# Optimization experiments

Hardware: AMD Instinct MI355X
Metric: run time of the kernel (lower is better)

Reference implementation:

```python
import jax, jax.numpy as jnp
import numpy as np

TRIANGLE_TABLE = jnp.array([
    [-1,-1,-1,-1,-1,-1],[1,0,2,-1,-1,-1],[4,0,3,-1,-1,-1],[1,4,2,1,3,4],
    [3,1,5,-1,-1,-1],[2,3,0,2,5,3],[1,4,0,1,5,4],[4,2,5,-1,-1,-1],
    [4,5,2,-1,-1,-1],[4,1,0,4,5,1],[3,2,0,3,5,2],[1,3,5,-1,-1,-1],
    [4,1,2,4,3,1],[3,0,4,-1,-1,-1],[2,0,1,-1,-1,-1],[-1,-1,-1,-1,-1,-1]], dtype=jnp.int32)
NUM_TRI_TABLE = jnp.array([0,1,1,2,1,2,2,1,1,2,2,1,2,1,1,0], dtype=jnp.int32)
BASE_TET_EDGES = jnp.array([0,1,0,2,0,3,1,2,1,3,2,3], dtype=jnp.int32)
N_VERTS, N_TETS = 200_000, 1_000_000


def setup_inputs() -> dict:
    key = jax.random.key(0)
    k1, k2, k3 = jax.random.split(key, 3)
    pos_nx3 = jax.random.normal(k1, (N_VERTS, 3), jnp.float32)
    sdf_n = jax.random.normal(k2, (N_VERTS,), jnp.float32)
    tet_fx4 = jax.random.randint(k3, (N_TETS, 4), 0, N_VERTS, dtype=jnp.int32)
    return {"pos_nx3": pos_nx3, "sdf_n": sdf_n, "tet_fx4": tet_fx4}


def _mt_indices(sdf_n, tet_fx4):
    # Index-only part (torch.no_grad in the original). Dynamic shapes -> eager jax.
    occ_n = sdf_n > 0                              # [N]
    occ_fx4 = occ_n[tet_fx4]                       # [T,4]
    occ_sum = occ_fx4.sum(-1)
    valid = (occ_sum > 0) & (occ_sum < 4)          # surface-crossing tets
    tets_v = tet_fx4[valid]                        # [Tv,4]
    occ_v = occ_fx4[valid]
    # 6 edges per tet, sorted so (min,max) -> dedup identical to torch sort_edges+unique
    all_edges = jnp.sort(tets_v[:, BASE_TET_EDGES].reshape(-1, 2), axis=1)  # [Tv*6,2]
    unique_edges, idx_map = jnp.unique(all_edges, axis=0, return_inverse=True)
    idx_map = idx_map.reshape(-1)
    mask_edges = occ_n[unique_edges].sum(-1) == 1  # exactly one endpoint inside
    # compacting map: -1 for non-crossing edges, running index for crossing ones
    mapping = jnp.where(mask_edges, jnp.cumsum(mask_edges.astype(jnp.int32)) - 1, -1)
    idx_map = mapping[idx_map].reshape(-1, 6)      # [Tv,6] per-tet edge->vertex ids
    interp_v = unique_edges[mask_edges]            # [Ne,2] endpoint indices
    return valid, occ_v, idx_map, interp_v


def _interp_verts(pos, sdf, interp_v):
    e_pos = pos[interp_v]                                   # [Ne,2,3]
    e_sdf = sdf[interp_v] * jnp.array([1.0, -1.0], sdf.dtype)  # [s0,-s1]
    denom = e_sdf.sum(1, keepdims=True)                     # s0 - s1
    w = e_sdf[:, ::-1] / denom                              # [-s1, s0] / (s0-s1)
    return (e_pos * w[..., None]).sum(1)                    # [Ne,3]


def _map_uv(face_gidx, max_idx):
    Ngrid = int(np.ceil(np.sqrt((max_idx + 1) // 2)))
    lin = jnp.linspace(0.0, 1.0 - 1.0 / Ngrid, Ngrid, dtype=jnp.float32)
    tex_y, tex_x = jnp.meshgrid(lin, lin, indexing='ij')
    pad = 0.9 / Ngrid
    uvs = jnp.stack([tex_x, tex_y, tex_x + pad, tex_y,
                     tex_x + pad, tex_y + pad, tex_x, tex_y + pad], axis=-1).reshape(-1, 2)
    tet_raw = face_gidx // 2
    tet_idx = (tet_raw // Ngrid) * Ngrid + tet_raw % Ngrid
    tri_idx = face_gidx % 2
    uv_idx = jnp.stack([tet_idx * 4, tet_idx * 4 + tri_idx + 1,
                        tet_idx * 4 + tri_idx + 2], axis=-1).reshape(-1, 3)
    return uvs, uv_idx


def reference(pos_nx3, sdf_n, tet_fx4):
    valid, occ_v, idx_map, interp_v = _mt_indices(sdf_n, tet_fx4)
    verts = _interp_verts(pos_nx3, sdf_n, interp_v)
    # triangle-table lookup
    v_id = jnp.array([1, 2, 4, 8], jnp.int32)
    tetindex = (occ_v.astype(jnp.int32) * v_id).sum(-1)     # [Tv]
    num_tri = NUM_TRI_TABLE[tetindex]
    m1, m2 = num_tri == 1, num_tri == 2
    faces1 = jnp.take_along_axis(idx_map[m1], TRIANGLE_TABLE[tetindex[m1]][:, :3], axis=1).reshape(-1, 3)
    faces2 = jnp.take_along_axis(idx_map[m2], TRIANGLE_TABLE[tetindex[m2]][:, :6], axis=1).reshape(-1, 3)
    faces = jnp.concatenate([faces1, faces2], axis=0)
    tet_gidx = jnp.nonzero(valid)[0].astype(jnp.int32)
    face_gidx = jnp.concatenate([
        tet_gidx[m1] * 2,
        jnp.stack([tet_gidx[m2] * 2, tet_gidx[m2] * 2 + 1], axis=-1).reshape(-1)], axis=0)
    uvs, uv_idx = _map_uv(face_gidx, tet_fx4.shape[0] * 2)
    return verts, faces, uvs, uv_idx
```

## Files before the change

kernel.cpp:

```cpp
#include <hip/hip_runtime.h>
#include <cmath>

typedef unsigned long long u64;
typedef unsigned int u32;
typedef unsigned char u8;

#define SCAN_BLOCK 256
#define SCAN_ELEMS 8
#define SCAN_TILE (SCAN_BLOCK * SCAN_ELEMS)

#define BIN_SHIFT 9
#define BIN_VR 512
#define TETS_PER_BLOCK 2048

__constant__ int d_NUMTRI[16] = {0,1,1,2,1,2,2,1,1,2,2,1,2,1,1,0};
__constant__ int d_TRI[16][6] = {
 {-1,-1,-1,-1,-1,-1},{1,0,2,-1,-1,-1},{4,0,3,-1,-1,-1},{1,4,2,1,3,4},
 {3,1,5,-1,-1,-1},{2,3,0,2,5,3},{1,4,0,1,5,4},{4,2,5,-1,-1,-1},
 {4,5,2,-1,-1,-1},{4,1,0,4,5,1},{3,2,0,3,5,2},{1,3,5,-1,-1,-1},
 {4,1,2,4,3,1},{3,0,4,-1,-1,-1},{2,0,1,-1,-1,-1},{-1,-1,-1,-1,-1,-1}};
__constant__ int d_E0[6] = {0,0,0,1,1,2};
__constant__ int d_E1[6] = {1,2,3,2,3,3};

template <typename T>
__global__ void scanA_t(const T* in, T* out, int n, T* blockSums) {
    __shared__ T tsum[SCAN_BLOCK];
    int tbase = blockIdx.x * SCAN_TILE + threadIdx.x * SCAN_ELEMS;
    T vals[SCAN_ELEMS];
    T run = 0;
    for (int k = 0; k < SCAN_ELEMS; ++k) {
        int i = tbase + k;
        T v = (i < n) ? in[i] : (T)0;
        vals[k] = run;
        run += v;
    }
    tsum[threadIdx.x] = run;
    __syncthreads();
    for (int off = 1; off < SCAN_BLOCK; off <<= 1) {
        T v = (threadIdx.x >= (unsigned)off) ? tsum[threadIdx.x - off] : (T)0;
        __syncthreads();
        tsum[threadIdx.x] += v;
        __syncthreads();
    }
    T texcl = (threadIdx.x == 0) ? (T)0 : tsum[threadIdx.x - 1];
    for (int k = 0; k < SCAN_ELEMS; ++k) {
        int i = tbase + k;
        if (i < n) out[i] = texcl + vals[k];
    }
    if (threadIdx.x == SCAN_BLOCK - 1) blockSums[blockIdx.x] = tsum[SCAN_BLOCK - 1];
}

template <typename T>
__global__ void scanB_t(T* bs, int nb, T* totalOut) {
    __shared__ T sh[2048];
    for (int i = threadIdx.x; i < 2048; i += 256) sh[i] = (i < nb) ? bs[i] : (T)0;
    __syncthreads();
    for (int off = 1; off < 2048; off <<= 1) {
        T v[8];
        for (int k = 0; k < 8; ++k) {
            int i = threadIdx.x + k * 256;
            v[k] = (i >= off) ? sh[i - off] : (T)0;
        }
        __syncthreads();
        for (int k = 0; k < 8; ++k) sh[threadIdx.x + k * 256] += v[k];
        __syncthreads();
    }
    for (int i = threadIdx.x; i < nb; i += 256) bs[i] = (i == 0) ? (T)0 : sh[i - 1];
    if (threadIdx.x == 0 && totalOut) *totalOut = (nb > 0) ? sh[nb - 1] : (T)0;
}

template <typename T>
__global__ void scanC_t(T* out, int n, const T* bs) {
    int base = blockIdx.x * SCAN_TILE;
    T add = bs[blockIdx.x];
    int end = base + SCAN_TILE; if (end > n) end = n;
    for (int i = base + threadIdx.x; i < end; i += SCAN_BLOCK) out[i] += add;
}

__global__ __launch_bounds__(256) void k_classify_hist(
    const int* tet, const float* sdf, u8* ti8, u64* tetPack,
    u32* blockHist, int T, int NB, int gB) {
    __shared__ u32 hist[BIN_VR];
    for (int i = threadIdx.x; i < NB; i += 256) hist[i] = 0;
    __syncthreads();
    int base = blockIdx.x * TETS_PER_BLOCK;
    for (int it = 0; it < TETS_PER_BLOCK / 256; ++it) {
        int t = base + it * 256 + threadIdx.x;
        if (t < T) {
            int4 q = reinterpret_cast<const int4*>(tet)[t];
            int ti = (sdf[q.x] > 0.0f ? 1 : 0) | (sdf[q.y] > 0.0f ? 2 : 0) |
                     (sdf[q.z] > 0.0f ? 4 : 0) | (sdf[q.w] > 0.0f ? 8 : 0);
            ti8[t] = (u8)ti;
            int nt = d_NUMTRI[ti];
            tetPack[t] = ((u64)(nt == 1 ? 1 : 0) << 21) | (u64)(nt == 2 ? 1 : 0);
            if (nt != 0) {
                int idx[4] = {q.x, q.y, q.z, q.w};
                #pragma unroll
                for (int e = 0; e < 6; ++e) {
                    int e0 = d_E0[e], e1 = d_E1[e];
                    if (((ti >> e0) ^ (ti >> e1)) & 1) {
                        int a = idx[e0], b = idx[e1];
                        int mn = a < b ? a : b;
                        atomicAdd(&hist[mn >> BIN_SHIFT], 1u);
                    }
                }
            }
        }
    }
    __syncthreads();
    for (int i = threadIdx.x; i < NB; i += 256)
        blockHist[(size_t)i * gB + blockIdx.x] = hist[i];
}

__global__ __launch_bounds__(256) void k_binfill(
    const int* tet, const u8* ti8, const u32* blockHistScan,
    u32* binData, int T, int NB, int gB) {
    __shared__ u32 cur[BIN_VR];
    for (int i = threadIdx.x; i < NB; i += 256)
        cur[i] = blockHistScan[(size_t)i * gB + blockIdx.x];
    __syncthreads();
    int base = blockIdx.x * TETS_PER_BLOCK;
    for (int it = 0; it < TETS_PER_BLOCK / 256; ++it) {
        int t = base + it * 256 + threadIdx.x;
        if (t < T) {
            int ti = ti8[t];
            if (d_NUMTRI[ti] != 0) {
                int4 q = reinterpret_cast<const int4*>(tet)[t];
                int idx[4] = {q.x, q.y, q.z, q.w};
                #pragma unroll
                for (int e = 0; e < 6; ++e) {
                    int e0 = d_E0[e], e1 = d_E1[e];
                    if (((ti >> e0) ^ (ti >> e1)) & 1) {
                        int a = idx[e0], b = idx[e1];
                        int mn = a < b ? a : b;
                        int mx = a < b ? b : a;
                        u32 slot = atomicAdd(&cur[mn >> BIN_SHIFT], 1u);
                        binData[slot] = ((u32)(mn & (BIN_VR - 1)) << 18) | (u32)mx;
                    }
                }
            }
        }
    }
}

__global__ __launch_bounds__(256) void k_bincount(
    const u32* blockHistScan, const u32* totalPtr, const u32* binData,
    u32* bucketCnt, u32* padCnt, int V, int NB, int gB) {
    int bin = blockIdx.x;
    __shared__ u32 hist[BIN_VR];
    for (int i = threadIdx.x; i < BIN_VR; i += 256) hist[i] = 0;
    __syncthreads();
    u32 s = blockHistScan[(size_t)bin * gB];
    u32 e = (bin + 1 < NB) ? blockHistScan[(size_t)(bin + 1) * gB] : *totalPtr;
    for (u32 i = s + threadIdx.x; i < e; i += 256)
        atomicAdd(&hist[binData[i] >> 18], 1u);
    __syncthreads();
    int vbase = bin << BIN_SHIFT;
    for (int i = threadIdx.x; i < BIN_VR; i += 256) {
        int v = vbase + i;
        if (v < V) {
            u32 h = hist[i];
            bucketCnt[v] = h;
            padCnt[v] = (h + 15u) & ~15u;
        }
    }
}

__global__ __launch_bounds__(256) void k_binscatter(
    const u32* blockHistScan, const u32* totalPtr, const u32* binData,
    const u32* bucketStart, u32* maxArr, int V, int NB, int gB) {
    int bin = blockIdx.x;
    __shared__ u32 cur[BIN_VR];
    int vbase = bin << BIN_SHIFT;
    for (int i = threadIdx.x; i < BIN_VR; i += 256) {
        int v = vbase + i;
        cur[i] = (v < V) ? bucketStart[v] : 0u;
    }
    __syncthreads();
    u32 s = blockHistScan[(size_t)bin * gB];
    u32 e = (bin + 1 < NB) ? blockHistScan[(size_t)(bin + 1) * gB] : *totalPtr;
    for (u32 i = s + threadIdx.x; i < e; i += 256) {
        u32 rec = binData[i];
        u32 slot = atomicAdd(&cur[rec >> 18], 1u);
        maxArr[slot] = rec & 0x3FFFFu;
    }
}

__global__ __launch_bounds__(64) void k_sortdedup(
    const u32* bucketCnt, const u32* bucketStart, u32* maxArr, u32* crossCnt, int V)
{
    int v = blockIdx.x;
    if (v >= V) return;
    int lane = threadIdx.x;
    int n = (int)bucketCnt[v];
    if (n == 0) { if (lane == 0) crossCnt[v] = 0; return; }
    long long start = (long long)bucketStart[v];

    if (n <= 64) {
        u32 key = (lane < n) ? maxArr[start + lane] : 0xFFFFFFFFu;
        int rank = 0;
        for (int j = 0; j < n; ++j) {
            u32 kj = (u32)__shfl((int)key, j);
            rank += (kj < key || (kj == key && j < lane)) ? 1 : 0;
        }
        u32 sorted = (u32)__builtin_amdgcn_ds_permute(rank << 2, (int)key);
        u32 prev = (u32)__shfl((int)sorted, lane - 1);
        bool nf = (lane < n) && (lane == 0 || prev != sorted);
        u64 m = __ballot(nf);
        int idx = __popcll(m & ((1ull << lane) - 1ull));
        if (nf) maxArr[start + idx] = sorted;
        if (lane == 0) crossCnt[v] = (u32)__popcll(m);
    } else if (n <= 256) {
        __shared__ u32 sk[256];
        __shared__ u32 ss[256];
        int chunks = (n + 63) >> 6;
        u32 key[4];
        #pragma unroll
        for (int c = 0; c < 4; ++c) {
            if (c < chunks) {
                int i = (c << 6) + lane;
                key[c] = (i < n) ? maxArr[start + i] : 0xFFFFFFFFu;
                sk[(c << 6) + lane] = key[c];
            }
        }
        __syncthreads();
        int rank[4] = {0, 0, 0, 0};
        for (int j = 0; j < n; ++j) {
            u32 kj = sk[j];
            #pragma unroll
            for (int c = 0; c < 4; ++c) {
                if (c < chunks) {
                    int i = (c << 6) + lane;
                    rank[c] += (kj < key[c] || (kj == key[c] && j < i)) ? 1 : 0;
                }
            }
        }
        #pragma unroll
        for (int c = 0; c < 4; ++c) {
            if (c < chunks) { int i = (c << 6) + lane; if (i < n) ss[rank[c]] = key[c]; }
        }
        __syncthreads();
        int carryU = 0;
        for (int c = 0; c < chunks; ++c) {
            int i = (c << 6) + lane;
            bool valid = i < n;
            u32 k = ss[i < 256 ? i : 255];
            bool nf = valid && (i == 0 || ss[i - 1] != k);
            u64 mnf = __ballot(nf);
            u64 incl = (2ull << lane) - 1ull;
            int uIncl = carryU + __popcll(mnf & incl);
            if (nf) maxArr[start + uIncl - 1] = k;
            carryU += __popcll(mnf);
        }
        if (lane == 0) crossCnt[v] = (u32)carryU;
    } else if (lane == 0) {
        for (int i = 1; i < n; ++i) {
            u32 kk = maxArr[start + i];
            int j = i - 1;
            while (j >= 0 && maxArr[start + j] > kk) {
                maxArr[start + j + 1] = maxArr[start + j]; --j;
            }
            maxArr[start + j + 1] = kk;
        }
        int uc = 0; u32 prev = 0xFFFFFFFFu;
        for (int i = 0; i < n; ++i) {
            u32 k = maxArr[start + i];
            if (k != prev) { maxArr[start + uc] = k; ++uc; prev = k; }
        }
        crossCnt[v] = (u32)uc;
    }
}

__global__ void k_metapack(const u32* bucketStart, const u32* crossCnt,
                           const u32* crossScan, uint2* meta2, int V) {
    int v = blockIdx.x * 256 + threadIdx.x;
    if (v < V) meta2[v] = make_uint2(bucketStart[v], (crossCnt[v] << 22) | crossScan[v]);
}

__global__ __launch_bounds__(64) void k_verts(
    const u32* crossCnt, const u32* bucketStart, const u32* maxArr, const u32* crossScan,
    const float* pos, const float* sdf, float* out, int V)
{
    int v = blockIdx.x;
    if (v >= V) return;
    int lane = threadIdx.x;
    int u = (int)crossCnt[v];
    if (u == 0) return;
    long long start = (long long)bucketStart[v];
    int cBase = (int)crossScan[v];
    float s0 = sdf[v];
    float p0x = pos[3 * v], p0y = pos[3 * v + 1], p0z = pos[3 * v + 2];
    for (int i = lane; i < u; i += 64) {
        int b = (int)maxArr[start + i];
        long long k = cBase + i;
        float s1 = sdf[b];
        float d = s0 - s1;
        float w0 = -s1 / d, w1 = s0 / d;
        out[3 * k + 0] = p0x * w0 + pos[3 * b + 0] * w1;
        out[3 * k + 1] = p0y * w0 + pos[3 * b + 1] * w1;
        out[3 * k + 2] = p0z * w0 + pos[3 * b + 2] * w1;
    }
}

__global__ void k_faces(const int* tet, const u8* ti8, const u64* tetScan,
                        const uint2* meta2, const u32* maxArr,
                        const u64* meta0, const u32* NePtr,
                        float* out, int T, int Ngrid, long long uvFloats)
{
    int t = blockIdx.x * 256 + threadIdx.x;
    if (t >= T) return;
    int ti = ti8[t];
    int nt = d_NUMTRI[ti];
    if (nt == 0) return;

    u64 tot = *meta0;
    int C1 = (int)((tot >> 21) & 0x1fffffull);
    int C2 = (int)(tot & 0x1fffffull);
    int Ne = (int)*NePtr;
    long long facesBase = 3LL * Ne;
    long long F = (long long)C1 + 2LL * C2;
    long long uvIdxBase = facesBase + 3LL * F + uvFloats;

    int4 q = reinterpret_cast<const int4*>(tet)[t];
    int idx[4] = {q.x, q.y, q.z, q.w};
    const int* row = d_TRI[ti];

    int emap[6];
    unsigned done = 0;
    float fv[6];
    #pragma unroll
    for (int j = 0; j < 6; ++j) {
        if (j >= 3 * nt) break;
        int e = row[j];
        if (!((done >> e) & 1)) {
            done |= 1u << e;
            int a = idx[d_E0[e]], b = idx[d_E1[e]];
            if (a > b) { int tmp = a; a = b; b = tmp; }
            uint2 m = meta2[a];
            int u = (int)(m.y >> 22);
            int base = (int)(m.y & 0x3FFFFFu);
            const uint4* bp = (const uint4*)(maxArr + m.x);
            int cnt = 0;
            int nv = (u + 3) >> 2;
            for (int k4 = 0; k4 < nv; ++k4) {
                uint4 w = bp[k4];
                int b4 = k4 << 2;
                cnt += (b4 + 0 < u && (int)w.x < b) ? 1 : 0;
                cnt += (b4 + 1 < u && (int)w.y < b) ? 1 : 0;
                cnt += (b4 + 2 < u && (int)w.z < b) ? 1 : 0;
                cnt += (b4 + 3 < u && (int)w.w < b) ? 1 : 0;
            }
            emap[e] = base + cnt;
        }
        fv[j] = (float)emap[e];
    }

    u64 sc = tetScan[t];
    int r1 = (int)((sc >> 21) & 0x1fffffull);
    int r2 = (int)(sc & 0x1fffffull);
    int tet_idx = (t / Ngrid) * Ngrid + (t % Ngrid);

    if (nt == 1) {
        long long f = r1;
        out[facesBase + 3 * f + 0] = fv[0];
        out[facesBase + 3 * f + 1] = fv[1];
        out[facesBase + 3 * f + 2] = fv[2];
        out[uvIdxBase + 3 * f + 0] = (float)(4 * tet_idx);
        out[uvIdxBase + 3 * f + 1] = (float)(4 * tet_idx + 1);
        out[uvIdxBase + 3 * f + 2] = (float)(4 * tet_idx + 2);
    } else {
        long long f0 = (long long)C1 + 2LL * r2;
        out[facesBase + 3 * f0 + 0] = fv[0];
        out[facesBase + 3 * f0 + 1] = fv[1];
        out[facesBase + 3 * f0 + 2] = fv[2];
        out[facesBase + 3 * (f0 + 1) + 0] = fv[3];
        out[facesBase + 3 * (f0 + 1) + 1] = fv[4];
        out[facesBase + 3 * (f0 + 1) + 2] = fv[5];
        out[uvIdxBase + 3 * f0 + 0] = (float)(4 * tet_idx);
        out[uvIdxBase + 3 * f0 + 1] = (float)(4 * tet_idx + 1);
        out[uvIdxBase + 3 * f0 + 2] = (float)(4 * tet_idx + 2);
        out[uvIdxBase + 3 * (f0 + 1) + 0] = (float)(4 * tet_idx);
        out[uvIdxBase + 3 * (f0 + 1) + 1] = (float)(4 * tet_idx + 2);
        out[uvIdxBase + 3 * (f0 + 1) + 2] = (float)(4 * tet_idx + 3);
    }
}

__global__ void k_uvs(float* out, const u64* meta0, const u32* NePtr, int Ngrid) {
    int c = blockIdx.x * 256 + threadIdx.x;
    int total = Ngrid * Ngrid;
    if (c >= total) return;
    u64 tot = *meta0;
    int C1 = (int)((tot >> 21) & 0x1fffffull);
    int C2 = (int)(tot & 0x1fffffull);
    int Ne = (int)*NePtr;
    long long uvBase = 3LL * Ne + 3LL * ((long long)C1 + 2LL * C2);
    int i = c / Ngrid, j = c % Ngrid;
    double step = (Ngrid > 1) ? (1.0 - 1.0 / (double)Ngrid) / (double)(Ngrid - 1) : 0.0;
    float x = (float)((double)j * step);
    float y = (float)((double)i * step);
    float pad = (float)(0.9 / (double)Ngrid);
    long long o = uvBase + 8LL * c;
    out[o + 0] = x;       out[o + 1] = y;
    out[o + 2] = x + pad; out[o + 3] = y;
    out[o + 4] = x + pad; out[o + 5] = y + pad;
    out[o + 6] = x;       out[o + 7] = y + pad;
}

template <typename T>
static void run_scan_t(const T* in, T* out, int n, T* blockSums, T* totalOut,
                       hipStream_t stream) {
    int nb = (n + SCAN_TILE - 1) / SCAN_TILE;
    scanA_t<T><<<nb, SCAN_BLOCK, 0, stream>>>(in, out, n, blockSums);
    scanB_t<T><<<1, 256, 0, stream>>>(blockSums, nb, totalOut);
    scanC_t<T><<<nb, SCAN_BLOCK, 0, stream>>>(out, n, blockSums);
}

extern "C" void kernel_launch(void* const* d_in, const int* in_sizes, int n_in,
                              void* d_out, int out_size, void* d_ws, size_t ws_size,
                              hipStream_t stream) {
    const float* pos = (const float*)d_in[0];
    const float* sdf = (const float*)d_in[1];
    const int* tet = (const int*)d_in[2];
    int V = in_sizes[1];
    int T = in_sizes[2] / 4;
    float* out = (float*)d_out;

    int NB = (V + BIN_VR - 1) / BIN_VR;
    int gB = (T + TETS_PER_BLOCK - 1) / TETS_PER_BLOCK;
    int nHist = NB * gB;

    char* p = (char*)d_ws;
    auto alloc = [&](size_t bytes) -> void* {
        void* r = (void*)p;
        p += (bytes + 255) & ~(size_t)255;
        return r;
    };
    u8*  ti8           = (u8*) alloc((size_t)T);
    u64* tetPack       = (u64*)alloc((size_t)T * 8);
    u64* tetScan       = (u64*)alloc((size_t)T * 8);
    u32* blockHist     = (u32*)alloc((size_t)nHist * 4);
    u32* blockHistScan = (u32*)alloc((size_t)nHist * 4);
    u32* binData       = (u32*)alloc((size_t)6 * T * 4);
    u32* bucketCnt     = (u32*)alloc((size_t)V * 4);
    u32* padCnt        = (u32*)alloc((size_t)V * 4);
    u32* bucketStart   = (u32*)alloc((size_t)V * 4);
    u32* crossCnt      = (u32*)alloc((size_t)V * 4);
    u32* crossScan     = (u32*)alloc((size_t)V * 4);
    uint2* meta2       = (uint2*)alloc((size_t)V * 8);
    u32* maxArr        = (u32*)alloc(((size_t)6 * T + 16 * (size_t)V) * 4);
    u64* blockSums64   = (u64*)alloc(2048 * 8);
    u32* blockSums32   = (u32*)alloc(2048 * 4);
    u64* meta64        = (u64*)alloc(8 * 8);
    u32* NePtr         = (u32*)(meta64 + 4);
    u32* NeInstPtr     = (u32*)(meta64 + 5);

    long long M = (2LL * T + 1) / 2;
    int Ngrid = (int)std::sqrt((double)M);
    while ((long long)Ngrid * Ngrid < M) ++Ngrid;
    if (Ngrid < 1) Ngrid = 1;
    long long uvFloats = 8LL * Ngrid * Ngrid;

    int gV = (V + 255) / 256;
    int gT = (T + 255) / 256;

    k_classify_hist<<<gB, 256, 0, stream>>>(tet, sdf, ti8, tetPack, blockHist,
                                            T, NB, gB);
    run_scan_t<u64>(tetPack, tetScan, T, blockSums64, meta64, stream);
    run_scan_t<u32>(blockHist, blockHistScan, nHist, blockSums32, NeInstPtr, stream);
    k_binfill<<<gB, 256, 0, stream>>>(tet, ti8, blockHistScan, binData, T, NB, gB);
    k_bincount<<<NB, 256, 0, stream>>>(blockHistScan, NeInstPtr, binData,
                                       bucketCnt, padCnt, V, NB, gB);
    run_scan_t<u32>(padCnt, bucketStart, V, blockSums32, nullptr, stream);
    k_binscatter<<<NB, 256, 0, stream>>>(blockHistScan, NeInstPtr, binData,
                                         bucketStart, maxArr, V, NB, gB);
    k_sortdedup<<<V, 64, 0, stream>>>(bucketCnt, bucketStart, maxArr, crossCnt, V);
    run_scan_t<u32>(crossCnt, crossScan, V, blockSums32, NePtr, stream);
    k_metapack<<<gV, 256, 0, stream>>>(bucketStart, crossCnt, crossScan, meta2, V);
    k_verts<<<V, 64, 0, stream>>>(crossCnt, bucketStart, maxArr, crossScan,
                                  pos, sdf, out, V);
    k_faces<<<gT, 256, 0, stream>>>(tet, ti8, tetScan, meta2, maxArr,
                                    meta64, NePtr, out, T, Ngrid, uvFloats);
    int gUV = (Ngrid * Ngrid + 255) / 256;
    k_uvs<<<gUV, 256, 0, stream>>>(out, meta64, NePtr, Ngrid);
}
```

Baseline: 500.5 us.

## Track edge provenance through binning to build direct per-tet edge index map

Each crossing edge record now carries a provenance id (tet*6+edge) through binfill and binscatter. The sort/dedup kernel uses it to write each edge's local unique index into an idxmap laid over the binData buffer. k_faces then reads the six entries per tet directly instead of linearly scanning each vertex's sorted bucket, and the metapack kernel is removed. In exchange it adds extra global writes and reads for provenance, scattered nontemporal stores, and raises the shared-sort path limit to 1024 elements with larger register arrays.

```diff
diff --git a/kernel.cpp b/kernel.cpp
--- a/kernel.cpp
+++ b/kernel.cpp
@@ -114,7 +114,7 @@
 
 __global__ __launch_bounds__(256) void k_binfill(
     const int* tet, const u8* ti8, const u32* blockHistScan,
-    u32* binData, int T, int NB, int gB) {
+    u32* binData, u32* binProv, int T, int NB, int gB) {
     __shared__ u32 cur[BIN_VR];
     for (int i = threadIdx.x; i < NB; i += 256)
         cur[i] = blockHistScan[(size_t)i * gB + blockIdx.x];
@@ -136,6 +136,7 @@
                         int mx = a < b ? b : a;
                         u32 slot = atomicAdd(&cur[mn >> BIN_SHIFT], 1u);
                         binData[slot] = ((u32)(mn & (BIN_VR - 1)) << 18) | (u32)mx;
+                        binProv[slot] = 6u * (u32)t + (u32)e;
                     }
                 }
             }
@@ -168,7 +169,8 @@
 
 __global__ __launch_bounds__(256) void k_binscatter(
     const u32* blockHistScan, const u32* totalPtr, const u32* binData,
-    const u32* bucketStart, u32* maxArr, int V, int NB, int gB) {
+    const u32* binProv, const u32* bucketStart, u32* maxArr, u32* provArr,
+    int V, int NB, int gB) {
     int bin = blockIdx.x;
     __shared__ u32 cur[BIN_VR];
     int vbase = bin << BIN_SHIFT;
@@ -181,13 +183,16 @@
     u32 e = (bin + 1 < NB) ? blockHistScan[(size_t)(bin + 1) * gB] : *totalPtr;
     for (u32 i = s + threadIdx.x; i < e; i += 256) {
         u32 rec = binData[i];
+        u32 pv = binProv[i];
         u32 slot = atomicAdd(&cur[rec >> 18], 1u);
         maxArr[slot] = rec & 0x3FFFFu;
+        provArr[slot] = pv;
     }
 }
 
 __global__ __launch_bounds__(64) void k_sortdedup(
-    const u32* bucketCnt, const u32* bucketStart, u32* maxArr, u32* crossCnt, int V)
+    const u32* bucketCnt, const u32* bucketStart, u32* maxArr,
+    u32* provArr, u32* idxmap, u32* crossCnt, int V)
 {
     int v = blockIdx.x;
     if (v >= V) return;
@@ -198,6 +203,7 @@
 
     if (n <= 64) {
         u32 key = (lane < n) ? maxArr[start + lane] : 0xFFFFFFFFu;
+        u32 prov = (lane < n) ? provArr[start + lane] : 0u;
         int rank = 0;
         for (int j = 0; j < n; ++j) {
             u32 kj = (u32)__shfl((int)key, j);
@@ -209,26 +215,32 @@
         u64 m = __ballot(nf);
         int idx = __popcll(m & ((1ull << lane) - 1ull));
         if (nf) maxArr[start + idx] = sorted;
+        int ldSorted = nf ? idx : idx - 1;
+        int ldOrig = __shfl(ldSorted, rank);
+        if (lane < n)
+            __builtin_nontemporal_store((u32)ldOrig, &idxmap[prov]);
         if (lane == 0) crossCnt[v] = (u32)__popcll(m);
-    } else if (n <= 256) {
-        __shared__ u32 sk[256];
-        __shared__ u32 ss[256];
+    } else if (n <= 1024) {
+        __shared__ u32 sk[1024];
+        __shared__ u32 ss[1024];
+        __shared__ u32 sdd[1024];
         int chunks = (n + 63) >> 6;
-        u32 key[4];
+        u32 key[16];
+        int rank[16];
         #pragma unroll
-        for (int c = 0; c < 4; ++c) {
+        for (int c = 0; c < 16; ++c) {
             if (c < chunks) {
                 int i = (c << 6) + lane;
                 key[c] = (i < n) ? maxArr[start + i] : 0xFFFFFFFFu;
                 sk[(c << 6) + lane] = key[c];
+                rank[c] = 0;
             }
         }
         __syncthreads();
-        int rank[4] = {0, 0, 0, 0};
         for (int j = 0; j < n; ++j) {
             u32 kj = sk[j];
             #pragma unroll
-            for (int c = 0; c < 4; ++c) {
+            for (int c = 0; c < 16; ++c) {
                 if (c < chunks) {
                     int i = (c << 6) + lane;
                     rank[c] += (kj < key[c] || (kj == key[c] && j < i)) ? 1 : 0;
@@ -236,7 +248,7 @@
             }
         }
         #pragma unroll
-        for (int c = 0; c < 4; ++c) {
+        for (int c = 0; c < 16; ++c) {
             if (c < chunks) { int i = (c << 6) + lane; if (i < n) ss[rank[c]] = key[c]; }
         }
         __syncthreads();
@@ -244,37 +256,48 @@
         for (int c = 0; c < chunks; ++c) {
             int i = (c << 6) + lane;
             bool valid = i < n;
-            u32 k = ss[i < 256 ? i : 255];
+            u32 k = ss[valid ? i : n - 1];
             bool nf = valid && (i == 0 || ss[i - 1] != k);
             u64 mnf = __ballot(nf);
             u64 incl = (2ull << lane) - 1ull;
             int uIncl = carryU + __popcll(mnf & incl);
             if (nf) maxArr[start + uIncl - 1] = k;
+            if (valid) sdd[i] = (u32)(uIncl - 1);
             carryU += __popcll(mnf);
+        }
+        __syncthreads();
+        #pragma unroll
+        for (int c = 0; c < 16; ++c) {
+            if (c < chunks) {
+                int i = (c << 6) + lane;
+                if (i < n)
+                    __builtin_nontemporal_store(sdd[rank[c]],
+                                                &idxmap[provArr[start + i]]);
+            }
         }
         if (lane == 0) crossCnt[v] = (u32)carryU;
     } else if (lane == 0) {
         for (int i = 1; i < n; ++i) {
             u32 kk = maxArr[start + i];
+            u32 pp = provArr[start + i];
             int j = i - 1;
             while (j >= 0 && maxArr[start + j] > kk) {
-                maxArr[start + j + 1] = maxArr[start + j]; --j;
+                maxArr[start + j + 1] = maxArr[start + j];
+                provArr[start + j + 1] = provArr[start + j];
+                --j;
             }
             maxArr[start + j + 1] = kk;
+            provArr[start + j + 1] = pp;
         }
         int uc = 0; u32 prev = 0xFFFFFFFFu;
         for (int i = 0; i < n; ++i) {
             u32 k = maxArr[start + i];
             if (k != prev) { maxArr[start + uc] = k; ++uc; prev = k; }
+            __builtin_nontemporal_store((u32)(uc - 1),
+                                        &idxmap[provArr[start + i]]);
         }
         crossCnt[v] = (u32)uc;
     }
-}
-
-__global__ void k_metapack(const u32* bucketStart, const u32* crossCnt,
-                           const u32* crossScan, uint2* meta2, int V) {
-    int v = blockIdx.x * 256 + threadIdx.x;
-    if (v < V) meta2[v] = make_uint2(bucketStart[v], (crossCnt[v] << 22) | crossScan[v]);
 }
 
 __global__ __launch_bounds__(64) void k_verts(
@@ -303,7 +326,7 @@
 }
 
 __global__ void k_faces(const int* tet, const u8* ti8, const u64* tetScan,
-                        const uint2* meta2, const u32* maxArr,
+                        const u32* idxmap, const u32* crossScan,
                         const u64* meta0, const u32* NePtr,
                         float* out, int T, int Ngrid, long long uvFloats)
 {
@@ -323,6 +346,9 @@
 
     int4 q = reinterpret_cast<const int4*>(tet)[t];
     int idx[4] = {q.x, q.y, q.z, q.w};
+    const uint2* imp = reinterpret_cast<const uint2*>(idxmap + 6ll * t);
+    uint2 r0 = imp[0], r1 = imp[1], r2 = imp[2];
+    u32 im[6] = {r0.x, r0.y, r1.x, r1.y, r2.x, r2.y};
     const int* row = d_TRI[ti];
 
     int emap[6];
@@ -335,33 +361,19 @@
         if (!((done >> e) & 1)) {
             done |= 1u << e;
             int a = idx[d_E0[e]], b = idx[d_E1[e]];
-            if (a > b) { int tmp = a; a = b; b = tmp; }
-            uint2 m = meta2[a];
-            int u = (int)(m.y >> 22);
-            int base = (int)(m.y & 0x3FFFFFu);
-            const uint4* bp = (const uint4*)(maxArr + m.x);
-            int cnt = 0;
-            int nv = (u + 3) >> 2;
-            for (int k4 = 0; k4 < nv; ++k4) {
-                uint4 w = bp[k4];
-                int b4 = k4 << 2;
-                cnt += (b4 + 0 < u && (int)w.x < b) ? 1 : 0;
-                cnt += (b4 + 1 < u && (int)w.y < b) ? 1 : 0;
-                cnt += (b4 + 2 < u && (int)w.z < b) ? 1 : 0;
-                cnt += (b4 + 3 < u && (int)w.w < b) ? 1 : 0;
-            }
-            emap[e] = base + cnt;
+            if (b < a) a = b;
+            emap[e] = (int)crossScan[a] + (int)im[e];
         }
         fv[j] = (float)emap[e];
     }
 
     u64 sc = tetScan[t];
-    int r1 = (int)((sc >> 21) & 0x1fffffull);
-    int r2 = (int)(sc & 0x1fffffull);
+    int r1s = (int)((sc >> 21) & 0x1fffffull);
+    int r2s = (int)(sc & 0x1fffffull);
     int tet_idx = (t / Ngrid) * Ngrid + (t % Ngrid);
 
     if (nt == 1) {
-        long long f = r1;
+        long long f = r1s;
         out[facesBase + 3 * f + 0] = fv[0];
         out[facesBase + 3 * f + 1] = fv[1];
         out[facesBase + 3 * f + 2] = fv[2];
@@ -369,7 +381,7 @@
         out[uvIdxBase + 3 * f + 1] = (float)(4 * tet_idx + 1);
         out[uvIdxBase + 3 * f + 2] = (float)(4 * tet_idx + 2);
     } else {
-        long long f0 = (long long)C1 + 2LL * r2;
+        long long f0 = (long long)C1 + 2LL * r2s;
         out[facesBase + 3 * f0 + 0] = fv[0];
         out[facesBase + 3 * f0 + 1] = fv[1];
         out[facesBase + 3 * f0 + 2] = fv[2];
@@ -441,44 +453,48 @@
     u32* blockHist     = (u32*)alloc((size_t)nHist * 4);
     u32* blockHistScan = (u32*)alloc((size_t)nHist * 4);
     u32* binData       = (u32*)alloc((size_t)6 * T * 4);
+    u32* binProv       = (u32*)alloc((size_t)6 * T * 4);
     u32* bucketCnt     = (u32*)alloc((size_t)V * 4);
     u32* padCnt        = (u32*)alloc((size_t)V * 4);
     u32* bucketStart   = (u32*)alloc((size_t)V * 4);
     u32* crossCnt      = (u32*)alloc((size_t)V * 4);
     u32* crossScan     = (u32*)alloc((size_t)V * 4);
-    uint2* meta2       = (uint2*)alloc((size_t)V * 8);
     u32* maxArr        = (u32*)alloc(((size_t)6 * T + 16 * (size_t)V) * 4);
+    u32* provArr       = (u32*)alloc(((size_t)6 * T + 16 * (size_t)V) * 4);
     u64* blockSums64   = (u64*)alloc(2048 * 8);
     u32* blockSums32   = (u32*)alloc(2048 * 4);
     u64* meta64        = (u64*)alloc(8 * 8);
     u32* NePtr         = (u32*)(meta64 + 4);
     u32* NeInstPtr     = (u32*)(meta64 + 5);
 
+    u32* idxmap = binData;
+
     long long M = (2LL * T + 1) / 2;
     int Ngrid = (int)std::sqrt((double)M);
     while ((long long)Ngrid * Ngrid < M) ++Ngrid;
     if (Ngrid < 1) Ngrid = 1;
     long long uvFloats = 8LL * Ngrid * Ngrid;
 
-    int gV = (V + 255) / 256;
     int gT = (T + 255) / 256;
 
     k_classify_hist<<<gB, 256, 0, stream>>>(tet, sdf, ti8, tetPack, blockHist,
                                             T, NB, gB);
     run_scan_t<u64>(tetPack, tetScan, T, blockSums64, meta64, stream);
     run_scan_t<u32>(blockHist, blockHistScan, nHist, blockSums32, NeInstPtr, stream);
-    k_binfill<<<gB, 256, 0, stream>>>(tet, ti8, blockHistScan, binData, T, NB, gB);
+    k_binfill<<<gB, 256, 0, stream>>>(tet, ti8, blockHistScan, binData, binProv,
+                                      T, NB, gB);
     k_bincount<<<NB, 256, 0, stream>>>(blockHistScan, NeInstPtr, binData,
                                        bucketCnt, padCnt, V, NB, gB);
     run_scan_t<u32>(padCnt, bucketStart, V, blockSums32, nullptr, stream);
     k_binscatter<<<NB, 256, 0, stream>>>(blockHistScan, NeInstPtr, binData,
-                                         bucketStart, maxArr, V, NB, gB);
-    k_sortdedup<<<V, 64, 0, stream>>>(bucketCnt, bucketStart, maxArr, crossCnt, V);
+                                         binProv, bucketStart, maxArr, provArr,
+                                         V, NB, gB);
+    k_sortdedup<<<V, 64, 0, stream>>>(bucketCnt, bucketStart, maxArr,
+                                      provArr, idxmap, crossCnt, V);
     run_scan_t<u32>(crossCnt, crossScan, V, blockSums32, NePtr, stream);
-    k_metapack<<<gV, 256, 0, stream>>>(bucketStart, crossCnt, crossScan, meta2, V);
     k_verts<<<V, 64, 0, stream>>>(crossCnt, bucketStart, maxArr, crossScan,
                                   pos, sdf, out, V);
-    k_faces<<<gT, 256, 0, stream>>>(tet, ti8, tetScan, meta2, maxArr,
+    k_faces<<<gT, 256, 0, stream>>>(tet, ti8, tetScan, idxmap, crossScan,
                                     meta64, NePtr, out, T, Ngrid, uvFloats);
     int gUV = (Ngrid * Ngrid + 255) / 256;
     k_uvs<<<gUV, 256, 0, stream>>>(out, meta64, NePtr, Ngrid);
```

Result: slower. 543.2 us (+8.5%).
